# Kernel optimization log

Measured on AMD Instinct MI355X. Metric: run time of the kernel, lower is better.

## Reference

```python
import jax, jax.numpy as jnp
from jax import lax
import numpy as np
from math import lgamma

N_MELS = 80; MEMORY_DIM = 512; PRENET = (256, 256)
ATTN_LSTM = 1024; ATTN_DIM = 128
N_STATIC = 8; SF = 21; N_DYN = 8; DF = 21
PRIOR_LEN = 11; ALPHA = 0.1; BETA = 0.9
DEC_LSTM = 1024; R = 2
B = 32; T_MELS = 800; T_ENC = 200


def _betabinom_pmf(k, n, a, b):
    lbeta = lambda x, y: lgamma(x) + lgamma(y) - lgamma(x + y)
    return np.exp(lgamma(n + 1) - lgamma(k + 1) - lgamma(n - k + 1) + lbeta(k + a, n - k + b) - lbeta(a, b))


def setup_inputs() -> dict:
    key = jax.random.key(0)
    ks = iter(jax.random.split(key, 40))
    w = lambda shape, s=0.05: jax.random.normal(next(ks), shape, jnp.float32) * s
    # prior filter, flipped as in the torch buffer (so cross-correlation == convolution with pmf)
    prior = np.array([_betabinom_pmf(k, PRIOR_LEN - 1, ALPHA, BETA) for k in range(PRIOR_LEN)], np.float32)[::-1].copy()
    return {
        "mels": w((B, N_MELS, T_MELS), 1.0),
        "memory": w((B, T_ENC, MEMORY_DIM), 1.0),
        "prenet_W1": w((PRENET[0], N_MELS)), "prenet_b1": jnp.zeros((PRENET[0],), jnp.float32),
        "prenet_W2": w((PRENET[1], PRENET[0])), "prenet_b2": jnp.zeros((PRENET[1],), jnp.float32),
        "attn_Wih": w((4 * ATTN_LSTM, PRENET[1] + MEMORY_DIM)), "attn_Whh": w((4 * ATTN_LSTM, ATTN_LSTM)),
        "attn_bih": jnp.zeros((4 * ATTN_LSTM,), jnp.float32), "attn_bhh": jnp.zeros((4 * ATTN_LSTM,), jnp.float32),
        "dca_Wq": w((ATTN_DIM, ATTN_LSTM)), "dca_bq": jnp.zeros((ATTN_DIM,), jnp.float32),
        "dca_V": w((N_DYN * DF, ATTN_DIM)),
        "dca_F": w((N_STATIC, 1, SF)),
        "dca_U": w((ATTN_DIM, N_STATIC)),
        "dca_T": w((ATTN_DIM, N_DYN)), "dca_Tb": jnp.zeros((ATTN_DIM,), jnp.float32),
        "dca_v": w((1, ATTN_DIM)),
        "prior": jnp.asarray(prior),
        "dec_Wih": w((4 * DEC_LSTM, ATTN_LSTM + MEMORY_DIM)), "dec_Whh": w((4 * DEC_LSTM, DEC_LSTM)),
        "dec_bih": jnp.zeros((4 * DEC_LSTM,), jnp.float32), "dec_bhh": jnp.zeros((4 * DEC_LSTM,), jnp.float32),
        "ac_W": w((N_MELS * R, DEC_LSTM + MEMORY_DIM)), "ac_b": jnp.zeros((N_MELS * R,), jnp.float32),
    }


def _lstm_cell(x, h, c, Wih, Whh, bih, bhh):
    g = x @ Wih.T + bih + h @ Whh.T + bhh
    i, f, gg, o = jnp.split(g, 4, axis=-1)  # torch gate order i,f,g,o
    c_new = jax.nn.sigmoid(f) * c + jax.nn.sigmoid(i) * jnp.tanh(gg)
    h_new = jax.nn.sigmoid(o) * jnp.tanh(c_new)
    return h_new, c_new


def _conv1d(x, k, pad, groups=1):
    # x: [B, Cin, T], k: [Cout, Cin/groups, K]; cross-correlation, like torch conv1d
    return lax.conv_general_dilated(x, k, (1,), [pad], feature_group_count=groups)


def _dca_step(query, memory, aw, prior, Wq, bq, V, Fk, U, Tw, Tb, v):
    Bsz, T = aw.shape
    # location prior: causal conv with (flipped) betabinom pmf
    p = _conv1d(aw[:, None, :], prior[None, None, :], (PRIOR_LEN - 1, 0))[:, 0, :]
    p = jnp.log(jnp.maximum(p, 1e-6))
    # dynamic filters predicted from query, applied per-batch via grouped conv
    G = jnp.tanh(query @ Wq.T + bq) @ V.T  # [B, N_DYN*DF]
    g = _conv1d(aw[None, :, :], G.reshape(Bsz * N_DYN, 1, DF), ((DF - 1) // 2, (DF - 1) // 2), groups=Bsz)
    g = g.reshape(Bsz, N_DYN, T).transpose(0, 2, 1)  # [B, T, N_DYN]
    # static location filters
    f = _conv1d(aw[:, None, :], Fk, ((SF - 1) // 2, (SF - 1) // 2)).transpose(0, 2, 1)  # [B, T, N_STATIC]
    e = (jnp.tanh(f @ U.T + g @ Tw.T + Tb) @ v.T)[:, :, 0] + p  # [B, T]
    aw_new = jax.nn.softmax(e, axis=-1)
    ctx = jnp.einsum("bt,btd->bd", aw_new, memory)
    return aw_new, ctx


def reference(mels, memory, prenet_W1, prenet_b1, prenet_W2, prenet_b2, attn_Wih, attn_Whh, attn_bih, attn_bhh, dca_Wq, dca_bq, dca_V, dca_F, dca_U, dca_T, dca_Tb, dca_v, prior, dec_Wih, dec_Whh, dec_bih, dec_bhh, ac_W, ac_b):
    Bsz, n_mels, T_mels = mels.shape
    T_enc = memory.shape[1]
    n_steps = T_mels // R
    go = jnp.zeros((Bsz, n_mels), mels.dtype)
    # teacher forcing: step t>0 consumes ground-truth frame at index t*R - 1
    tf = mels[:, :, R - 1::R][:, :, : n_steps - 1].transpose(2, 0, 1)
    frames = jnp.concatenate([go[None], tf], axis=0)  # [S, B, n_mels]
    aw0 = jnp.zeros((Bsz, T_enc), mels.dtype).at[:, 0].set(1.0)  # one-hot init attention
    carry0 = (jnp.zeros((Bsz, MEMORY_DIM), mels.dtype),
              jnp.zeros((Bsz, ATTN_LSTM), mels.dtype), jnp.zeros((Bsz, ATTN_LSTM), mels.dtype),
              jnp.zeros((Bsz, DEC_LSTM), mels.dtype), jnp.zeros((Bsz, DEC_LSTM), mels.dtype),
              aw0)

    def step(carry, frame):
        ctx, ah, acs, dh, dcs, aw = carry
        x = jax.nn.relu(frame @ prenet_W1.T + prenet_b1)
        x = jax.nn.relu(x @ prenet_W2.T + prenet_b2)
        ah, acs = _lstm_cell(jnp.concatenate([ctx, x], -1), ah, acs, attn_Wih, attn_Whh, attn_bih, attn_bhh)
        aw, ctx = _dca_step(ah, memory, aw, prior, dca_Wq, dca_bq, dca_V, dca_F, dca_U, dca_T, dca_Tb, dca_v)
        dh, dcs = _lstm_cell(jnp.concatenate([ah, ctx], -1), dh, dcs, dec_Wih, dec_Whh, dec_bih, dec_bhh)
        out = jnp.concatenate([dh, ctx], -1) @ ac_W.T + ac_b  # [B, n_mels*R]
        return (ctx, ah, acs, dh, dcs, aw), (out, aw)

    _, (outs, aws) = lax.scan(step, carry0, frames)
    # per-step [B, n_mels, R] frames concatenated along time (step-major)
    output_mels = outs.reshape(n_steps, Bsz, n_mels, R).transpose(1, 2, 0, 3).reshape(Bsz, n_mels, n_steps * R)
    alignments = aws.transpose(1, 2, 0)  # [B, T_enc, n_steps]
    return output_mels, alignments
```

## Files before the change

kernel.cpp:

```cpp
#include <hip/hip_runtime.h>
#include <hip/hip_bf16.h>

typedef unsigned short u16;
typedef unsigned int   u32;

#define NTHR 256

#define BATCH 32
#define TENC  200
#define NMELS 80
#define TMELS 800
#define NSTEP 400

#define OFF_AH    0
#define OFF_ACS   65536
#define OFF_DH    98304
#define OFF_DCS   131072
#define OFF_CTX   163840
#define OFF_AW    180224
#define OFF_FBUF  186624
#define OFF_PBUF  237824
#define OFF_GPART 244224
#define OFF_X     375296
#define FLOAT_END 3652096
#define ZERO_CNT  180224

#define B_AWIH 0
#define B_AWHH 3145728
#define B_DWIH 7340032
#define B_DWHH 13631488
#define B_ACW  17825792
#define B_WQ   18071552
#define B_MEMT 18202624

struct KArgs {
  const float *mels, *memory, *pW1, *pb1, *pW2, *pb2;
  const float *aWih, *aWhh, *abih, *abhh;
  const float *Wq, *bq, *V, *F, *U, *T, *Tb, *vv, *prior;
  const float *dWih, *dWhh, *dbih, *dbhh, *acW, *acb;
  float *out;
  float *ws;
  u16   *wb;
};

__device__ __forceinline__ float sigf(float x) {
  x = fminf(fmaxf(x, -30.f), 30.f);
  return 1.0f / (1.0f + __expf(-x));
}
__device__ __forceinline__ float ftanh(float x) {
  x = fminf(fmaxf(x, -15.f), 15.f);
  float e = __expf(2.f * x);
  return (e - 1.f) / (e + 1.f);
}
__device__ __forceinline__ float blo(u32 u) {
  union { u32 i; float f; } v; v.i = u << 16; return v.f;
}
__device__ __forceinline__ float bhi(u32 u) {
  union { u32 i; float f; } v; v.i = u & 0xffff0000u; return v.f;
}
__device__ __forceinline__ u16 f2b(float x) {
  __hip_bfloat16 h = __float2bfloat16(x);
  return *reinterpret_cast<u16*>(&h);
}

__device__ __forceinline__ void loadx(const float* src, float* xin) {
  const float4* p = (const float4*)src;
  #pragma unroll
  for (int q = 0; q < 8; ++q) {
    float4 v = p[q];
    xin[q*4+0] = v.x; xin[q*4+1] = v.y; xin[q*4+2] = v.z; xin[q*4+3] = v.w;
  }
}

__device__ __forceinline__ float dot32b(const float* xin, const u16* w) {
  const uint4* wp = (const uint4*)w;
  float acc = 0.f;
  #pragma unroll
  for (int q = 0; q < 4; ++q) {
    uint4 wv = wp[q];
    acc += blo(wv.x)*xin[q*8+0] + bhi(wv.x)*xin[q*8+1]
         + blo(wv.y)*xin[q*8+2] + bhi(wv.y)*xin[q*8+3]
         + blo(wv.z)*xin[q*8+4] + bhi(wv.z)*xin[q*8+5]
         + blo(wv.w)*xin[q*8+6] + bhi(wv.w)*xin[q*8+7];
  }
  return acc;
}

__device__ __forceinline__ float reduce8(float* smred, const float* acc) {
  const int t = threadIdx.x;
  const int b = t & 31, seg = t >> 5;
  __syncthreads();
  #pragma unroll
  for (int r = 0; r < 8; ++r) smred[(seg*8 + r)*32 + b] = acc[r];
  __syncthreads();
  const int r2 = t >> 5, b2 = t & 31;
  float tot = 0.f;
  #pragma unroll
  for (int sgi = 0; sgi < 8; ++sgi) tot += smred[(sgi*8 + r2)*32 + b2];
  return tot;
}

__device__ __forceinline__ void outproj(const KArgs& a, float* smred,
                                        const float* dh, const float* ctx,
                                        int pb, int sprev) {
  const int tid = threadIdx.x;
  const int b = tid & 31, seg = tid >> 5;
  const u16* wb = a.wb;
  float acc[8];
  #pragma unroll
  for (int r = 0; r < 8; ++r) acc[r] = 0.f;
  #pragma unroll 2
  for (int kc = 0; kc < 6; ++kc) {
    const float* src = (kc < 4) ? (dh + b*1024 + kc*256) : (ctx + b*512 + (kc-4)*256);
    float xin[32];
    loadx(src + seg*32, xin);
    #pragma unroll
    for (int r = 0; r < 8; ++r) {
      const int rr = pb*8 + r;
      acc[r] += dot32b(xin, wb + B_ACW + rr*1536 + kc*256 + seg*32);
    }
  }
  float tot = reduce8(smred, acc);
  const int r2 = tid >> 5, b2 = tid & 31;
  const int rr = pb*8 + r2;
  tot += a.acb[rr];
  a.out[(b2*NMELS + (rr >> 1))*TMELS + sprev*2 + (rr & 1)] = tot;
}

__global__ __launch_bounds__(NTHR) void init_kernel(KArgs a) {
  const int gtid = blockIdx.x*NTHR + threadIdx.x;
  const int str = gridDim.x*NTHR;
  float* ws = a.ws;
  for (int i = gtid; i < ZERO_CNT; i += str) ws[i] = 0.f;
  float* aw = ws + OFF_AW;
  for (int i = gtid; i < BATCH*TENC; i += str) aw[i] = ((i % TENC) == 0) ? 1.f : 0.f;
}

__global__ __launch_bounds__(NTHR) void conv_kernel(KArgs a) {
  const int gtid = blockIdx.x*NTHR + threadIdx.x;
  const int str = gridDim.x*NTHR;
  u16* wb = a.wb;
  for (int i = gtid; i < 3145728; i += str) wb[B_AWIH + i] = f2b(a.aWih[i]);
  for (int i = gtid; i < 4194304; i += str) wb[B_AWHH + i] = f2b(a.aWhh[i]);
  for (int i = gtid; i < 6291456; i += str) wb[B_DWIH + i] = f2b(a.dWih[i]);
  for (int i = gtid; i < 4194304; i += str) wb[B_DWHH + i] = f2b(a.dWhh[i]);
  for (int i = gtid; i < 245760;  i += str) wb[B_ACW  + i] = f2b(a.acW[i]);
  for (int i = gtid; i < 131072;  i += str) wb[B_WQ   + i] = f2b(a.Wq[i]);
  for (int i = gtid; i < 3276800; i += str) {
    const int b = i / 102400, rem = i - b*102400;
    const int d = rem / 200, t = rem - d*200;
    wb[B_MEMT + i] = f2b(a.memory[b*102400 + t*512 + d]);
  }
}

__global__ __launch_bounds__(NTHR) void prenet_kernel(KArgs a) {
  __shared__ float sm[384];
  const int tid = threadIdx.x;
  const int pair = blockIdx.x;
  const int s = pair >> 5, b = pair & 31;
  float* X = a.ws + OFF_X;
  if (tid < 80) {
    float v = 0.f;
    if (s > 0) v = a.mels[(b*NMELS + tid)*TMELS + 2*s - 1];
    sm[tid] = v;
  }
  __syncthreads();
  float a1 = a.pb1[tid];
  #pragma unroll 4
  for (int k = 0; k < 80; ++k) a1 += a.pW1[tid*80 + k] * sm[k];
  a1 = fmaxf(a1, 0.f);
  __syncthreads();
  sm[128 + tid] = a1;
  __syncthreads();
  float a2 = a.pb2[tid];
  #pragma unroll 4
  for (int k = 0; k < 256; ++k) a2 += a.pW2[tid*256 + k] * sm[128 + k];
  a2 = fmaxf(a2, 0.f);
  X[(s*BATCH + b)*256 + tid] = a2;
}

__device__ __forceinline__ void dca_step(const KArgs& a, float* sm, int b, int s,
                                         const float* ah_new, float* aw,
                                         const float* fbuf, const float* pbuf, float* ctx) {
  const int tid = threadIdx.x;
  const u16* wb = a.wb;
  float* s_ah  = sm;
  float* s_awp = sm + 1024;
  float* s_q   = sm + 1248;
  float* s_G   = sm + 1376;
  float* s_e   = sm + 1552;
  float* s_gg  = sm + 1760;
  float* s_ff  = sm + 3360;
  float* s_red = sm + 4960;
  float* s_awn = sm + 5216;
  for (int i = tid; i < 1024; i += NTHR) s_ah[i] = ah_new[b*1024 + i];
  if (tid < 220) s_awp[tid] = (tid >= 10 && tid < 210) ? aw[b*TENC + tid - 10] : 0.f;
  for (int i = tid; i < 1600; i += NTHR) s_ff[i] = fbuf[b*1600 + i];
  __syncthreads();
  {
    const int o = tid & 127, half = tid >> 7;
    const uint4* wq = (const uint4*)(wb + B_WQ + o*1024 + half*512);
    const float* xa = s_ah + half*512;
    float p = 0.f;
    #pragma unroll 8
    for (int q8 = 0; q8 < 64; ++q8) {
      uint4 w = wq[q8];
      const float* xq = xa + q8*8;
      p += blo(w.x)*xq[0] + bhi(w.x)*xq[1] + blo(w.y)*xq[2] + bhi(w.y)*xq[3]
         + blo(w.z)*xq[4] + bhi(w.z)*xq[5] + blo(w.w)*xq[6] + bhi(w.w)*xq[7];
    }
    s_red[tid] = p;
  }
  __syncthreads();
  if (tid < 128) s_q[tid] = ftanh(s_red[tid] + s_red[128 + tid] + a.bq[tid]);
  __syncthreads();
  if (tid < 168) {
    const float4* vp = (const float4*)(a.V + tid*128);
    float p = 0.f;
    #pragma unroll
    for (int q4 = 0; q4 < 32; ++q4) {
      float4 w = vp[q4];
      const float* xq = s_q + q4*4;
      p += w.x*xq[0] + w.y*xq[1] + w.z*xq[2] + w.w*xq[3];
    }
    s_G[tid] = p;
  }
  __syncthreads();
  for (int idx = tid; idx < 1600; idx += NTHR) {
    const int pos = idx >> 3, d = idx & 7;
    float p = 0.f;
    #pragma unroll
    for (int tau = 0; tau < 21; ++tau) p += s_awp[pos + tau] * s_G[d*21 + tau];
    s_gg[idx] = p;
  }
  __syncthreads();
  #pragma unroll 1
  for (int ro = 0; ro < 4; ++ro) {
    const int pos = ro*64 + (tid >> 2), sub = tid & 3;
    float av = 0.f;
    if (pos < 200) {
      const float* fpos = s_ff + pos*8;
      const float* gpos = s_gg + pos*8;
      #pragma unroll 4
      for (int fi = 0; fi < 32; ++fi) {
        const int ff = sub*32 + fi;
        const float4* Up = (const float4*)(a.U + ff*8);
        const float4* Tp = (const float4*)(a.T + ff*8);
        float4 u0 = Up[0], u1 = Up[1], t0 = Tp[0], t1 = Tp[1];
        float h = a.Tb[ff];
        h += u0.x*fpos[0] + u0.y*fpos[1] + u0.z*fpos[2] + u0.w*fpos[3]
           + u1.x*fpos[4] + u1.y*fpos[5] + u1.z*fpos[6] + u1.w*fpos[7];
        h += t0.x*gpos[0] + t0.y*gpos[1] + t0.z*gpos[2] + t0.w*gpos[3]
           + t1.x*gpos[4] + t1.y*gpos[5] + t1.z*gpos[6] + t1.w*gpos[7];
        av += a.vv[ff] * ftanh(h);
      }
    }
    av += __shfl_xor(av, 1);
    av += __shfl_xor(av, 2);
    if (sub == 0 && pos < 200) s_e[pos] = av + pbuf[b*TENC + pos];
  }
  __syncthreads();
  float mval = (tid < 200) ? s_e[tid] : -1e30f;
  #pragma unroll
  for (int off = 32; off > 0; off >>= 1) mval = fmaxf(mval, __shfl_xor(mval, off));
  if ((tid & 63) == 0) s_red[tid >> 6] = mval;
  __syncthreads();
  const float m = fmaxf(fmaxf(s_red[0], s_red[1]), fmaxf(s_red[2], s_red[3]));
  const float ex = (tid < 200) ? __expf(s_e[tid] - m) : 0.f;
  float sv = ex;
  #pragma unroll
  for (int off = 32; off > 0; off >>= 1) sv += __shfl_xor(sv, off);
  if ((tid & 63) == 0) s_red[4 + (tid >> 6)] = sv;
  __syncthreads();
  const float inv = 1.f / (s_red[4] + s_red[5] + s_red[6] + s_red[7]);
  if (tid < 200) {
    const float awv = ex * inv;
    aw[b*TENC + tid] = awv;
    s_awn[tid] = awv;
    a.out[2048000 + b*80000 + tid*400 + s] = awv;
  }
  __syncthreads();
  #pragma unroll 1
  for (int d = tid; d < 512; d += NTHR) {
    const uint4* mp = (const uint4*)(wb + B_MEMT + b*102400 + d*200);
    float p = 0.f;
    #pragma unroll 5
    for (int q = 0; q < 25; ++q) {
      uint4 v = mp[q];
      const float* aa = s_awn + q*8;
      p += blo(v.x)*aa[0] + bhi(v.x)*aa[1] + blo(v.y)*aa[2] + bhi(v.y)*aa[3]
         + blo(v.z)*aa[4] + bhi(v.z)*aa[5] + blo(v.w)*aa[6] + bhi(v.w)*aa[7];
    }
    ctx[b*512 + d] = p;
  }
}

__global__ __launch_bounds__(NTHR) void p1_kernel(KArgs a, int s) {
  __shared__ float sm[2560];
  float* smred = sm;
  float* smg   = sm + 2048;
  const int tid = threadIdx.x;
  const int bid = blockIdx.x;
  float* ws = a.ws;
  const u16* wb = a.wb;
  float* ah_prev = ws + OFF_AH + ((s & 1) ? 32768 : 0);
  float* ah_new  = ws + OFF_AH + ((s & 1) ? 0 : 32768);
  float* acs = ws + OFF_ACS;
  float* dh  = ws + OFF_DH;
  float* ctx = ws + OFF_CTX;
  float* aw  = ws + OFF_AW;
  float* fbuf  = ws + OFF_FBUF;
  float* pbuf  = ws + OFF_PBUF;
  float* gpart = ws + OFF_GPART;
  float* X     = ws + OFF_X;

  if (bid < 512) {
    const int b = tid & 31, seg = tid >> 5, u0 = bid*2;
    const float* Xs = X + s*BATCH*256;
    float acc[8];
    #pragma unroll
    for (int r = 0; r < 8; ++r) acc[r] = 0.f;
    #pragma unroll 2
    for (int kc = 0; kc < 7; ++kc) {
      const float* src = (kc < 2)  ? (ctx + b*512 + kc*256)
                       : (kc == 2) ? (Xs + b*256)
                                   : (ah_prev + b*1024 + (kc-3)*256);
      float xin[32];
      loadx(src + seg*32, xin);
      #pragma unroll
      for (int r = 0; r < 8; ++r) {
        const int rr = (r>>1)*1024 + u0 + (r&1);
        const u16* wr = (kc < 3) ? (wb + B_AWIH + rr*768 + kc*256 + seg*32)
                                 : (wb + B_AWHH + rr*1024 + (kc-3)*256 + seg*32);
        acc[r] += dot32b(xin, wr);
      }
    }
    float tot = reduce8(smred, acc);
    {
      const int r2 = tid >> 5, b2 = tid & 31;
      const int rr = (r2>>1)*1024 + u0 + (r2&1);
      smg[r2*32 + b2] = tot + a.abih[rr] + a.abhh[rr];
    }
    __syncthreads();
    if (tid < 64) {
      const int u = tid >> 5, b2 = tid & 31;
      const int j = u0 + u;
      const float gi = smg[(0+u)*32+b2], gf = smg[(2+u)*32+b2];
      const float gg = smg[(4+u)*32+b2], go = smg[(6+u)*32+b2];
      const float c = sigf(gf)*acs[b2*1024+j] + sigf(gi)*ftanh(gg);
      acs[b2*1024+j] = c;
      ah_new[b2*1024+j] = sigf(go)*ftanh(c);
    }
  } else if (bid < 1024) {
    const int b = tid & 31, seg = tid >> 5, j2 = bid - 512;
    float acc[8];
    #pragma unroll
    for (int r = 0; r < 8; ++r) acc[r] = 0.f;
    #pragma unroll 2
    for (int kc = 0; kc < 4; ++kc) {
      float xin[32];
      loadx(dh + b*1024 + kc*256 + seg*32, xin);
      #pragma unroll
      for (int r = 0; r < 8; ++r) {
        const int rr = j2*8 + r;
        acc[r] += dot32b(xin, wb + B_DWHH + rr*1024 + kc*256 + seg*32);
      }
    }
    float tot = reduce8(smred, acc);
    const int r2 = tid >> 5, b2 = tid & 31;
    const int rr = j2*8 + r2;
    gpart[rr*32 + b2] = tot + a.dbih[rr] + a.dbhh[rr];
  } else if (bid < 1044) {
    if (s > 0) outproj(a, smred, dh, ctx, bid - 1024, s - 1);
  } else {
    const int b4 = bid - 1044;
    if (tid < 224) sm[tid] = (tid >= 10 && tid < 210) ? aw[b4*TENC + tid - 10] : 0.f;
    __syncthreads();
    if (tid < 200) {
      #pragma unroll
      for (int j = 0; j < 8; ++j) {
        float p = 0.f;
        #pragma unroll
        for (int tau = 0; tau < 21; ++tau) p += sm[tid + tau] * a.F[j*21 + tau];
        fbuf[(b4*TENC + tid)*8 + j] = p;
      }
      float pp = 0.f;
      #pragma unroll
      for (int tau = 0; tau < 11; ++tau) pp += sm[tid + tau] * a.prior[tau];
      pbuf[b4*TENC + tid] = __logf(fmaxf(pp, 1e-6f));
    }
  }
}

__global__ __launch_bounds__(NTHR) void p2_kernel(KArgs a, int s) {
  __shared__ float sm[5536];
  const int tid = threadIdx.x;
  const int bid = blockIdx.x;
  float* ws = a.ws;
  const u16* wb = a.wb;
  float* ah_new = ws + OFF_AH + ((s & 1) ? 0 : 32768);
  float* ctx = ws + OFF_CTX;
  float* aw  = ws + OFF_AW;
  float* fbuf  = ws + OFF_FBUF;
  float* pbuf  = ws + OFF_PBUF;
  float* gpart = ws + OFF_GPART;

  if (bid < 32) {
    dca_step(a, sm, bid, s, ah_new, aw, fbuf, pbuf, ctx);
  } else {
    const int b = tid & 31, seg = tid >> 5, job = bid - 32;
    float acc[8];
    #pragma unroll
    for (int r = 0; r < 8; ++r) acc[r] = 0.f;
    #pragma unroll 2
    for (int kc = 0; kc < 4; ++kc) {
      float xin[32];
      loadx(ah_new + b*1024 + kc*256 + seg*32, xin);
      #pragma unroll
      for (int r = 0; r < 8; ++r) {
        const int rr = job*8 + r;
        acc[r] += dot32b(xin, wb + B_DWIH + rr*1536 + kc*256 + seg*32);
      }
    }
    float tot = reduce8(sm, acc);
    const int r2 = tid >> 5, b2 = tid & 31;
    const int rr = job*8 + r2;
    gpart[rr*32 + b2] += tot;
  }
}

__global__ __launch_bounds__(NTHR) void p3_kernel(KArgs a, int s) {
  __shared__ float sm[2560];
  float* smred = sm;
  float* smg   = sm + 2048;
  const int tid = threadIdx.x;
  const int bid = blockIdx.x;
  float* ws = a.ws;
  const u16* wb = a.wb;
  float* dh  = ws + OFF_DH;
  float* dcs = ws + OFF_DCS;
  float* ctx = ws + OFF_CTX;
  float* gpart = ws + OFF_GPART;

  const int b = tid & 31, seg = tid >> 5, u0 = bid*2;
  float acc[8];
  #pragma unroll
  for (int r = 0; r < 8; ++r) acc[r] = 0.f;
  #pragma unroll 2
  for (int kc = 0; kc < 2; ++kc) {
    float xin[32];
    loadx(ctx + b*512 + kc*256 + seg*32, xin);
    #pragma unroll
    for (int r = 0; r < 8; ++r) {
      const int rr = (r>>1)*1024 + u0 + (r&1);
      acc[r] += dot32b(xin, wb + B_DWIH + rr*1536 + 1024 + kc*256 + seg*32);
    }
  }
  float tot = reduce8(smred, acc);
  {
    const int r2 = tid >> 5, b2 = tid & 31;
    const int rr = (r2>>1)*1024 + u0 + (r2&1);
    smg[r2*32 + b2] = tot + gpart[rr*32 + b2];
  }
  __syncthreads();
  if (tid < 64) {
    const int u = tid >> 5, b2 = tid & 31;
    const int j = u0 + u;
    const float gi = smg[(0+u)*32+b2], gf = smg[(2+u)*32+b2];
    const float gg = smg[(4+u)*32+b2], go = smg[(6+u)*32+b2];
    const float c = sigf(gf)*dcs[b2*1024+j] + sigf(gi)*ftanh(gg);
    dcs[b2*1024+j] = c;
    dh[b2*1024+j] = sigf(go)*ftanh(c);
  }
}

__global__ __launch_bounds__(NTHR) void ep_kernel(KArgs a) {
  __shared__ float sm[2048];
  float* ws = a.ws;
  outproj(a, sm, ws + OFF_DH, ws + OFF_CTX, blockIdx.x, NSTEP - 1);
}

extern "C" void kernel_launch(void* const* d_in, const int* in_sizes, int n_in,
                              void* d_out, int out_size, void* d_ws, size_t ws_size,
                              hipStream_t stream) {
  (void)in_sizes; (void)n_in; (void)out_size; (void)ws_size;
  KArgs a;
  a.mels   = (const float*)d_in[0];
  a.memory = (const float*)d_in[1];
  a.pW1 = (const float*)d_in[2];  a.pb1 = (const float*)d_in[3];
  a.pW2 = (const float*)d_in[4];  a.pb2 = (const float*)d_in[5];
  a.aWih = (const float*)d_in[6]; a.aWhh = (const float*)d_in[7];
  a.abih = (const float*)d_in[8]; a.abhh = (const float*)d_in[9];
  a.Wq = (const float*)d_in[10];  a.bq = (const float*)d_in[11];
  a.V  = (const float*)d_in[12];  a.F  = (const float*)d_in[13];
  a.U  = (const float*)d_in[14];  a.T  = (const float*)d_in[15];
  a.Tb = (const float*)d_in[16];  a.vv = (const float*)d_in[17];
  a.prior = (const float*)d_in[18];
  a.dWih = (const float*)d_in[19]; a.dWhh = (const float*)d_in[20];
  a.dbih = (const float*)d_in[21]; a.dbhh = (const float*)d_in[22];
  a.acW  = (const float*)d_in[23]; a.acb  = (const float*)d_in[24];
  a.out = (float*)d_out;
  a.ws  = (float*)((char*)d_ws + 256);
  a.wb  = (u16*)(a.ws + FLOAT_END);

  hipLaunchKernelGGL(init_kernel, dim3(512), dim3(NTHR), 0, stream, a);
  hipLaunchKernelGGL(conv_kernel, dim3(2048), dim3(NTHR), 0, stream, a);
  hipLaunchKernelGGL(prenet_kernel, dim3(NSTEP*BATCH), dim3(NTHR), 0, stream, a);
  for (int s = 0; s < NSTEP; ++s) {
    hipLaunchKernelGGL(p1_kernel, dim3(1076), dim3(NTHR), 0, stream, a, s);
    hipLaunchKernelGGL(p2_kernel, dim3(544), dim3(NTHR), 0, stream, a, s);
    hipLaunchKernelGGL(p3_kernel, dim3(512), dim3(NTHR), 0, stream, a, s);
  }
  hipLaunchKernelGGL(ep_kernel, dim3(20), dim3(NTHR), 0, stream, a);
}
```

Before: 62.51 ms.

## Replace per-step kernel launches with persistent loop kernel using grid barriers

Replaces the 1200 per-step kernel launches (three phases per decoder step) with a single persistent kernel of 512 blocks that synchronizes through a global atomic barrier, two barriers per step. Work is regrouped so the attention-LSTM for step s+1 runs in the same phase as the decoder-LSTM finish for step s. ctx is double-buffered to make that overlap safe, and the decoder recurrent and attention-input gate products are merged into one job. This removes launch and kernel-boundary overhead. In exchange it relies on all 512 blocks being co-resident, and it has a spin barrier with a bail-out timeout.

```diff
diff --git a/kernel.cpp b/kernel.cpp
--- a/kernel.cpp
+++ b/kernel.cpp
@@ -5,6 +5,7 @@
 typedef unsigned int   u32;
 
 #define NTHR 256
+#define NBLK 512
 
 #define BATCH 32
 #define TENC  200
@@ -17,13 +18,13 @@
 #define OFF_DH    98304
 #define OFF_DCS   131072
 #define OFF_CTX   163840
-#define OFF_AW    180224
-#define OFF_FBUF  186624
-#define OFF_PBUF  237824
-#define OFF_GPART 244224
-#define OFF_X     375296
-#define FLOAT_END 3652096
-#define ZERO_CNT  180224
+#define OFF_AW    196608
+#define OFF_FBUF  203008
+#define OFF_PBUF  254208
+#define OFF_GPART 260608
+#define OFF_X     391680
+#define FLOAT_END 3668480
+#define ZERO_CNT  196608
 
 #define B_AWIH 0
 #define B_AWHH 3145728
@@ -41,6 +42,7 @@
   float *out;
   float *ws;
   u16   *wb;
+  int   *bar;
 };
 
 __device__ __forceinline__ float sigf(float x) {
@@ -61,6 +63,27 @@
 __device__ __forceinline__ u16 f2b(float x) {
   __hip_bfloat16 h = __float2bfloat16(x);
   return *reinterpret_cast<u16*>(&h);
+}
+
+__device__ __forceinline__ void gbar(int* bar, bool& bailed) {
+  __syncthreads();
+  if (threadIdx.x == 0 && !bailed) {
+    __threadfence();
+    int g = __hip_atomic_load(&bar[1], __ATOMIC_RELAXED, __HIP_MEMORY_SCOPE_AGENT);
+    int a = __hip_atomic_fetch_add(&bar[0], 1, __ATOMIC_ACQ_REL, __HIP_MEMORY_SCOPE_AGENT);
+    if (a == NBLK - 1) {
+      __hip_atomic_store(&bar[0], 0, __ATOMIC_RELAXED, __HIP_MEMORY_SCOPE_AGENT);
+      __hip_atomic_store(&bar[1], g + 1, __ATOMIC_RELEASE, __HIP_MEMORY_SCOPE_AGENT);
+    } else {
+      int it = 0;
+      while (__hip_atomic_load(&bar[1], __ATOMIC_ACQUIRE, __HIP_MEMORY_SCOPE_AGENT) == g) {
+        __builtin_amdgcn_s_sleep(1);
+        if (++it > (1 << 25)) { bailed = true; break; }
+      }
+    }
+    __threadfence();
+  }
+  __syncthreads();
 }
 
 __device__ __forceinline__ void loadx(const float* src, float* xin) {
@@ -125,58 +148,6 @@
   const int rr = pb*8 + r2;
   tot += a.acb[rr];
   a.out[(b2*NMELS + (rr >> 1))*TMELS + sprev*2 + (rr & 1)] = tot;
-}
-
-__global__ __launch_bounds__(NTHR) void init_kernel(KArgs a) {
-  const int gtid = blockIdx.x*NTHR + threadIdx.x;
-  const int str = gridDim.x*NTHR;
-  float* ws = a.ws;
-  for (int i = gtid; i < ZERO_CNT; i += str) ws[i] = 0.f;
-  float* aw = ws + OFF_AW;
-  for (int i = gtid; i < BATCH*TENC; i += str) aw[i] = ((i % TENC) == 0) ? 1.f : 0.f;
-}
-
-__global__ __launch_bounds__(NTHR) void conv_kernel(KArgs a) {
-  const int gtid = blockIdx.x*NTHR + threadIdx.x;
-  const int str = gridDim.x*NTHR;
-  u16* wb = a.wb;
-  for (int i = gtid; i < 3145728; i += str) wb[B_AWIH + i] = f2b(a.aWih[i]);
-  for (int i = gtid; i < 4194304; i += str) wb[B_AWHH + i] = f2b(a.aWhh[i]);
-  for (int i = gtid; i < 6291456; i += str) wb[B_DWIH + i] = f2b(a.dWih[i]);
-  for (int i = gtid; i < 4194304; i += str) wb[B_DWHH + i] = f2b(a.dWhh[i]);
-  for (int i = gtid; i < 245760;  i += str) wb[B_ACW  + i] = f2b(a.acW[i]);
-  for (int i = gtid; i < 131072;  i += str) wb[B_WQ   + i] = f2b(a.Wq[i]);
-  for (int i = gtid; i < 3276800; i += str) {
-    const int b = i / 102400, rem = i - b*102400;
-    const int d = rem / 200, t = rem - d*200;
-    wb[B_MEMT + i] = f2b(a.memory[b*102400 + t*512 + d]);
-  }
-}
-
-__global__ __launch_bounds__(NTHR) void prenet_kernel(KArgs a) {
-  __shared__ float sm[384];
-  const int tid = threadIdx.x;
-  const int pair = blockIdx.x;
-  const int s = pair >> 5, b = pair & 31;
-  float* X = a.ws + OFF_X;
-  if (tid < 80) {
-    float v = 0.f;
-    if (s > 0) v = a.mels[(b*NMELS + tid)*TMELS + 2*s - 1];
-    sm[tid] = v;
-  }
-  __syncthreads();
-  float a1 = a.pb1[tid];
-  #pragma unroll 4
-  for (int k = 0; k < 80; ++k) a1 += a.pW1[tid*80 + k] * sm[k];
-  a1 = fmaxf(a1, 0.f);
-  __syncthreads();
-  sm[128 + tid] = a1;
-  __syncthreads();
-  float a2 = a.pb2[tid];
-  #pragma unroll 4
-  for (int k = 0; k < 256; ++k) a2 += a.pW2[tid*256 + k] * sm[128 + k];
-  a2 = fmaxf(a2, 0.f);
-  X[(s*BATCH + b)*256 + tid] = a2;
 }
 
 __device__ __forceinline__ void dca_step(const KArgs& a, float* sm, int b, int s,
@@ -295,154 +266,103 @@
   }
 }
 
-__global__ __launch_bounds__(NTHR) void p1_kernel(KArgs a, int s) {
-  __shared__ float sm[2560];
+__device__ __forceinline__ void j1_job(const KArgs& a, float* sm, int s, int u0) {
   float* smred = sm;
   float* smg   = sm + 2048;
   const int tid = threadIdx.x;
-  const int bid = blockIdx.x;
   float* ws = a.ws;
   const u16* wb = a.wb;
-  float* ah_prev = ws + OFF_AH + ((s & 1) ? 32768 : 0);
-  float* ah_new  = ws + OFF_AH + ((s & 1) ? 0 : 32768);
+  float* ah_prev = ws + OFF_AH + (((s + 1) & 1) * 32768);
+  float* ah_new  = ws + OFF_AH + (((s) & 1) * 32768);
   float* acs = ws + OFF_ACS;
-  float* dh  = ws + OFF_DH;
-  float* ctx = ws + OFF_CTX;
-  float* aw  = ws + OFF_AW;
-  float* fbuf  = ws + OFF_FBUF;
-  float* pbuf  = ws + OFF_PBUF;
-  float* gpart = ws + OFF_GPART;
-  float* X     = ws + OFF_X;
-
-  if (bid < 512) {
-    const int b = tid & 31, seg = tid >> 5, u0 = bid*2;
-    const float* Xs = X + s*BATCH*256;
-    float acc[8];
-    #pragma unroll
-    for (int r = 0; r < 8; ++r) acc[r] = 0.f;
-    #pragma unroll 2
-    for (int kc = 0; kc < 7; ++kc) {
-      const float* src = (kc < 2)  ? (ctx + b*512 + kc*256)
-                       : (kc == 2) ? (Xs + b*256)
-                                   : (ah_prev + b*1024 + (kc-3)*256);
-      float xin[32];
-      loadx(src + seg*32, xin);
-      #pragma unroll
-      for (int r = 0; r < 8; ++r) {
-        const int rr = (r>>1)*1024 + u0 + (r&1);
-        const u16* wr = (kc < 3) ? (wb + B_AWIH + rr*768 + kc*256 + seg*32)
-                                 : (wb + B_AWHH + rr*1024 + (kc-3)*256 + seg*32);
-        acc[r] += dot32b(xin, wr);
-      }
-    }
-    float tot = reduce8(smred, acc);
-    {
-      const int r2 = tid >> 5, b2 = tid & 31;
-      const int rr = (r2>>1)*1024 + u0 + (r2&1);
-      smg[r2*32 + b2] = tot + a.abih[rr] + a.abhh[rr];
-    }
-    __syncthreads();
-    if (tid < 64) {
-      const int u = tid >> 5, b2 = tid & 31;
-      const int j = u0 + u;
-      const float gi = smg[(0+u)*32+b2], gf = smg[(2+u)*32+b2];
-      const float gg = smg[(4+u)*32+b2], go = smg[(6+u)*32+b2];
-      const float c = sigf(gf)*acs[b2*1024+j] + sigf(gi)*ftanh(gg);
-      acs[b2*1024+j] = c;
-      ah_new[b2*1024+j] = sigf(go)*ftanh(c);
-    }
-  } else if (bid < 1024) {
-    const int b = tid & 31, seg = tid >> 5, j2 = bid - 512;
-    float acc[8];
-    #pragma unroll
-    for (int r = 0; r < 8; ++r) acc[r] = 0.f;
-    #pragma unroll 2
-    for (int kc = 0; kc < 4; ++kc) {
-      float xin[32];
-      loadx(dh + b*1024 + kc*256 + seg*32, xin);
-      #pragma unroll
-      for (int r = 0; r < 8; ++r) {
-        const int rr = j2*8 + r;
-        acc[r] += dot32b(xin, wb + B_DWHH + rr*1024 + kc*256 + seg*32);
-      }
-    }
-    float tot = reduce8(smred, acc);
+  const float* ctxp = ws + OFF_CTX + (((s + 1) & 1) * 16384);
+  const float* Xs = ws + OFF_X + s * BATCH * 256;
+  const int b = tid & 31, seg = tid >> 5;
+  float acc[8];
+  #pragma unroll
+  for (int r = 0; r < 8; ++r) acc[r] = 0.f;
+  #pragma unroll 2
+  for (int kc = 0; kc < 7; ++kc) {
+    const float* src = (kc < 2)  ? (ctxp + b*512 + kc*256)
+                     : (kc == 2) ? (Xs + b*256)
+                                 : (ah_prev + b*1024 + (kc-3)*256);
+    float xin[32];
+    loadx(src + seg*32, xin);
+    #pragma unroll
+    for (int r = 0; r < 8; ++r) {
+      const int rr = (r>>1)*1024 + u0 + (r&1);
+      const u16* wr = (kc < 3) ? (wb + B_AWIH + rr*768 + kc*256 + seg*32)
+                               : (wb + B_AWHH + rr*1024 + (kc-3)*256 + seg*32);
+      acc[r] += dot32b(xin, wr);
+    }
+  }
+  float tot = reduce8(smred, acc);
+  {
     const int r2 = tid >> 5, b2 = tid & 31;
-    const int rr = j2*8 + r2;
-    gpart[rr*32 + b2] = tot + a.dbih[rr] + a.dbhh[rr];
-  } else if (bid < 1044) {
-    if (s > 0) outproj(a, smred, dh, ctx, bid - 1024, s - 1);
-  } else {
-    const int b4 = bid - 1044;
-    if (tid < 224) sm[tid] = (tid >= 10 && tid < 210) ? aw[b4*TENC + tid - 10] : 0.f;
-    __syncthreads();
-    if (tid < 200) {
-      #pragma unroll
-      for (int j = 0; j < 8; ++j) {
-        float p = 0.f;
-        #pragma unroll
-        for (int tau = 0; tau < 21; ++tau) p += sm[tid + tau] * a.F[j*21 + tau];
-        fbuf[(b4*TENC + tid)*8 + j] = p;
-      }
-      float pp = 0.f;
-      #pragma unroll
-      for (int tau = 0; tau < 11; ++tau) pp += sm[tid + tau] * a.prior[tau];
-      pbuf[b4*TENC + tid] = __logf(fmaxf(pp, 1e-6f));
-    }
-  }
-}
-
-__global__ __launch_bounds__(NTHR) void p2_kernel(KArgs a, int s) {
-  __shared__ float sm[5536];
-  const int tid = threadIdx.x;
-  const int bid = blockIdx.x;
+    const int rr = (r2>>1)*1024 + u0 + (r2&1);
+    smg[r2*32 + b2] = tot + a.abih[rr] + a.abhh[rr];
+  }
+  __syncthreads();
+  if (tid < 64) {
+    const int u = tid >> 5, b2 = tid & 31;
+    const int j = u0 + u;
+    const float gi = smg[(0+u)*32+b2], gf = smg[(2+u)*32+b2];
+    const float gg = smg[(4+u)*32+b2], go = smg[(6+u)*32+b2];
+    const float c = sigf(gf)*acs[b2*1024+j] + sigf(gi)*ftanh(gg);
+    acs[b2*1024+j] = c;
+    ah_new[b2*1024+j] = sigf(go)*ftanh(c);
+  }
+}
+
+__device__ __forceinline__ void jg_job(const KArgs& a, float* sm, int s, int g) {
+  const int tid = threadIdx.x;
+  const int b = tid & 31, seg = tid >> 5;
   float* ws = a.ws;
   const u16* wb = a.wb;
-  float* ah_new = ws + OFF_AH + ((s & 1) ? 0 : 32768);
-  float* ctx = ws + OFF_CTX;
-  float* aw  = ws + OFF_AW;
-  float* fbuf  = ws + OFF_FBUF;
-  float* pbuf  = ws + OFF_PBUF;
-  float* gpart = ws + OFF_GPART;
-
-  if (bid < 32) {
-    dca_step(a, sm, bid, s, ah_new, aw, fbuf, pbuf, ctx);
-  } else {
-    const int b = tid & 31, seg = tid >> 5, job = bid - 32;
-    float acc[8];
-    #pragma unroll
-    for (int r = 0; r < 8; ++r) acc[r] = 0.f;
-    #pragma unroll 2
-    for (int kc = 0; kc < 4; ++kc) {
-      float xin[32];
-      loadx(ah_new + b*1024 + kc*256 + seg*32, xin);
-      #pragma unroll
-      for (int r = 0; r < 8; ++r) {
-        const int rr = job*8 + r;
-        acc[r] += dot32b(xin, wb + B_DWIH + rr*1536 + kc*256 + seg*32);
-      }
-    }
-    float tot = reduce8(sm, acc);
+  const float* dh = ws + OFF_DH;
+  const float* ah = ws + OFF_AH + (((s) & 1) * 32768);
+  float acc[4];
+  #pragma unroll
+  for (int r = 0; r < 4; ++r) acc[r] = 0.f;
+  #pragma unroll 2
+  for (int kc = 0; kc < 8; ++kc) {
+    const float* src = (kc < 4) ? (dh + b*1024 + kc*256) : (ah + b*1024 + (kc-4)*256);
+    float xin[32];
+    loadx(src + seg*32, xin);
+    #pragma unroll
+    for (int r = 0; r < 4; ++r) {
+      const int rr = g*4 + r;
+      const u16* wr = (kc < 4) ? (wb + B_DWHH + rr*1024 + kc*256 + seg*32)
+                               : (wb + B_DWIH + rr*1536 + (kc-4)*256 + seg*32);
+      acc[r] += dot32b(xin, wr);
+    }
+  }
+  __syncthreads();
+  #pragma unroll
+  for (int r = 0; r < 4; ++r) sm[(seg*4 + r)*32 + b] = acc[r];
+  __syncthreads();
+  if (tid < 128) {
     const int r2 = tid >> 5, b2 = tid & 31;
-    const int rr = job*8 + r2;
-    gpart[rr*32 + b2] += tot;
-  }
-}
-
-__global__ __launch_bounds__(NTHR) void p3_kernel(KArgs a, int s) {
-  __shared__ float sm[2560];
+    const int rr = g*4 + r2;
+    float tot = 0.f;
+    #pragma unroll
+    for (int sgi = 0; sgi < 8; ++sgi) tot += sm[(sgi*4 + r2)*32 + b2];
+    ws[OFF_GPART + rr*32 + b2] = tot + a.dbih[rr] + a.dbhh[rr];
+  }
+}
+
+__device__ __forceinline__ void p3_job(const KArgs& a, float* sm, int s, int u0) {
   float* smred = sm;
   float* smg   = sm + 2048;
   const int tid = threadIdx.x;
-  const int bid = blockIdx.x;
   float* ws = a.ws;
   const u16* wb = a.wb;
   float* dh  = ws + OFF_DH;
   float* dcs = ws + OFF_DCS;
-  float* ctx = ws + OFF_CTX;
+  const float* ctx = ws + OFF_CTX + (((s) & 1) * 16384);
   float* gpart = ws + OFF_GPART;
 
-  const int b = tid & 31, seg = tid >> 5, u0 = bid*2;
+  const int b = tid & 31, seg = tid >> 5;
   float acc[8];
   #pragma unroll
   for (int r = 0; r < 8; ++r) acc[r] = 0.f;
@@ -474,10 +394,115 @@
   }
 }
 
-__global__ __launch_bounds__(NTHR) void ep_kernel(KArgs a) {
-  __shared__ float sm[2048];
+__device__ __forceinline__ void j4_job(const KArgs& a, float* sm, int b4) {
+  const int tid = threadIdx.x;
   float* ws = a.ws;
-  outproj(a, sm, ws + OFF_DH, ws + OFF_CTX, blockIdx.x, NSTEP - 1);
+  float* aw   = ws + OFF_AW;
+  float* fbuf = ws + OFF_FBUF;
+  float* pbuf = ws + OFF_PBUF;
+  __syncthreads();
+  if (tid < 224) sm[tid] = (tid >= 10 && tid < 210) ? aw[b4*TENC + tid - 10] : 0.f;
+  __syncthreads();
+  if (tid < 200) {
+    #pragma unroll
+    for (int j = 0; j < 8; ++j) {
+      float p = 0.f;
+      #pragma unroll
+      for (int tau = 0; tau < 21; ++tau) p += sm[tid + tau] * a.F[j*21 + tau];
+      fbuf[(b4*TENC + tid)*8 + j] = p;
+    }
+    float pp = 0.f;
+    #pragma unroll
+    for (int tau = 0; tau < 11; ++tau) pp += sm[tid + tau] * a.prior[tau];
+    pbuf[b4*TENC + tid] = __logf(fmaxf(pp, 1e-6f));
+  }
+}
+
+__global__ __launch_bounds__(NTHR) void init_kernel(KArgs a) {
+  const int gtid = blockIdx.x*NTHR + threadIdx.x;
+  const int str = gridDim.x*NTHR;
+  float* ws = a.ws;
+  if (gtid < 64) a.bar[gtid] = 0;
+  for (int i = gtid; i < ZERO_CNT; i += str) ws[i] = 0.f;
+  float* aw = ws + OFF_AW;
+  for (int i = gtid; i < BATCH*TENC; i += str) aw[i] = ((i % TENC) == 0) ? 1.f : 0.f;
+}
+
+__global__ __launch_bounds__(NTHR) void conv_kernel(KArgs a) {
+  const int gtid = blockIdx.x*NTHR + threadIdx.x;
+  const int str = gridDim.x*NTHR;
+  u16* wb = a.wb;
+  for (int i = gtid; i < 3145728; i += str) wb[B_AWIH + i] = f2b(a.aWih[i]);
+  for (int i = gtid; i < 4194304; i += str) wb[B_AWHH + i] = f2b(a.aWhh[i]);
+  for (int i = gtid; i < 6291456; i += str) wb[B_DWIH + i] = f2b(a.dWih[i]);
+  for (int i = gtid; i < 4194304; i += str) wb[B_DWHH + i] = f2b(a.dWhh[i]);
+  for (int i = gtid; i < 245760;  i += str) wb[B_ACW  + i] = f2b(a.acW[i]);
+  for (int i = gtid; i < 131072;  i += str) wb[B_WQ   + i] = f2b(a.Wq[i]);
+  for (int i = gtid; i < 3276800; i += str) {
+    const int b = i / 102400, rem = i - b*102400;
+    const int d = rem / 200, t = rem - d*200;
+    wb[B_MEMT + i] = f2b(a.memory[b*102400 + t*512 + d]);
+  }
+}
+
+__global__ __launch_bounds__(NTHR) void prenet_kernel(KArgs a) {
+  __shared__ float sm[384];
+  const int tid = threadIdx.x;
+  const int pair = blockIdx.x;
+  const int s = pair >> 5, b = pair & 31;
+  float* X = a.ws + OFF_X;
+  if (tid < 80) {
+    float v = 0.f;
+    if (s > 0) v = a.mels[(b*NMELS + tid)*TMELS + 2*s - 1];
+    sm[tid] = v;
+  }
+  __syncthreads();
+  float a1 = a.pb1[tid];
+  #pragma unroll 4
+  for (int k = 0; k < 80; ++k) a1 += a.pW1[tid*80 + k] * sm[k];
+  a1 = fmaxf(a1, 0.f);
+  __syncthreads();
+  sm[128 + tid] = a1;
+  __syncthreads();
+  float a2 = a.pb2[tid];
+  #pragma unroll 4
+  for (int k = 0; k < 256; ++k) a2 += a.pW2[tid*256 + k] * sm[128 + k];
+  a2 = fmaxf(a2, 0.f);
+  X[(s*BATCH + b)*256 + tid] = a2;
+}
+
+__global__ __launch_bounds__(NTHR, 2) void loop_kernel(KArgs a) {
+  __shared__ float sm[5536];
+  const int bid = blockIdx.x;
+  float* ws = a.ws;
+  int* bar = a.bar;
+  bool bailed = false;
+
+  j1_job(a, sm, 0, bid*2);
+  if (bid >= 480) j4_job(a, sm, bid - 480);
+  gbar(bar, bailed);
+
+  for (int s = 0; s < NSTEP; ++s) {
+    if (bid < 32) {
+      dca_step(a, sm, bid, s,
+               ws + OFF_AH  + (((s) & 1) * 32768),
+               ws + OFF_AW, ws + OFF_FBUF, ws + OFF_PBUF,
+               ws + OFF_CTX + (((s) & 1) * 16384));
+    } else if (bid < 52) {
+      if (s > 0) outproj(a, sm, ws + OFF_DH,
+                         ws + OFF_CTX + (((s - 1) & 1) * 16384), bid - 32, s - 1);
+    } else {
+      for (int g = bid - 52; g < 1024; g += (NBLK - 52)) jg_job(a, sm, s, g);
+    }
+    gbar(bar, bailed);
+    if (s + 1 < NSTEP) j1_job(a, sm, s + 1, bid*2);
+    p3_job(a, sm, s, bid*2);
+    if (bid >= 480 && s + 1 < NSTEP) j4_job(a, sm, bid - 480);
+    gbar(bar, bailed);
+  }
+
+  if (bid < 20) outproj(a, sm, ws + OFF_DH,
+                        ws + OFF_CTX + (((NSTEP - 1) & 1) * 16384), bid, NSTEP - 1);
 }
 
 extern "C" void kernel_launch(void* const* d_in, const int* in_sizes, int n_in,
@@ -500,16 +525,12 @@
   a.dbih = (const float*)d_in[21]; a.dbhh = (const float*)d_in[22];
   a.acW  = (const float*)d_in[23]; a.acb  = (const float*)d_in[24];
   a.out = (float*)d_out;
+  a.bar = (int*)d_ws;
   a.ws  = (float*)((char*)d_ws + 256);
   a.wb  = (u16*)(a.ws + FLOAT_END);
 
   hipLaunchKernelGGL(init_kernel, dim3(512), dim3(NTHR), 0, stream, a);
   hipLaunchKernelGGL(conv_kernel, dim3(2048), dim3(NTHR), 0, stream, a);
   hipLaunchKernelGGL(prenet_kernel, dim3(NSTEP*BATCH), dim3(NTHR), 0, stream, a);
-  for (int s = 0; s < NSTEP; ++s) {
-    hipLaunchKernelGGL(p1_kernel, dim3(1076), dim3(NTHR), 0, stream, a, s);
-    hipLaunchKernelGGL(p2_kernel, dim3(544), dim3(NTHR), 0, stream, a, s);
-    hipLaunchKernelGGL(p3_kernel, dim3(512), dim3(NTHR), 0, stream, a, s);
-  }
-  hipLaunchKernelGGL(ep_kernel, dim3(20), dim3(NTHR), 0, stream, a);
-}
+  hipLaunchKernelGGL(loop_kernel, dim3(NBLK), dim3(NTHR), 0, stream, a);
+}
```

After: 231.1 ms. +269.7%, slower.
